# Kernel optimization log

Measured on AMD Instinct MI355X. Metric: run time of the kernel, lower is better.

Reference implementation:

```python
import jax, jax.numpy as jnp
import numpy as np

N, E = 100000, 1600000
IN_C, HID, OUT = 128, 64, 25
EPS = 1e-5


def gcn_conv(x, row, col, W, b):
    # PyG GCNConv: h = x@W; add self-loops; sym-norm D^-1/2 A D^-1/2; + bias
    h = x @ W                                   # [N, F]
    ones = jnp.ones(row.shape[0], h.dtype)
    deg = jax.ops.segment_sum(ones, col, num_segments=N) + 1.0  # +1 self-loop
    dinv = jax.lax.rsqrt(deg)                   # [N]
    norm = dinv[row] * dinv[col]                # [E]
    agg = jax.ops.segment_sum(h[row] * norm[:, None], col, num_segments=N)
    agg = agg + (dinv * dinv)[:, None] * h      # self-loop contribution
    return agg + b


def layer_norm(x, w, b):
    # PyG LayerNorm mode='node': normalize each node over feature dim
    mu = jnp.mean(x, axis=-1, keepdims=True)
    var = jnp.var(x, axis=-1, keepdims=True)
    return (x - mu) * jax.lax.rsqrt(var + EPS) * w + b


def setup_inputs() -> dict:
    key = jax.random.key(0)
    ks = jax.random.split(key, 16)
    x = jax.random.normal(ks[0], (N, IN_C), dtype=jnp.float32)
    edge_index = jax.random.randint(ks[1], (2, E), 0, N, dtype=jnp.int32)

    def glorot(k, shp):
        lim = float(np.sqrt(6.0 / (shp[0] + shp[1])))
        return jax.random.uniform(k, shp, jnp.float32, -lim, lim)

    return {
        "x": x,
        "edge_index": edge_index,
        "W1": glorot(ks[2], (IN_C, HID)), "b1": jnp.zeros((HID,), jnp.float32),
        "W2": glorot(ks[3], (HID, HID)), "b2": jnp.zeros((HID,), jnp.float32),
        "W3": glorot(ks[4], (HID, HID)), "b3": jnp.zeros((HID,), jnp.float32),
        "ln1_w": jnp.ones((HID,), jnp.float32), "ln1_b": jnp.zeros((HID,), jnp.float32),
        "ln2_w": jnp.ones((HID,), jnp.float32), "ln2_b": jnp.zeros((HID,), jnp.float32),
        "ln3_w": jnp.ones((HID,), jnp.float32), "ln3_b": jnp.zeros((HID,), jnp.float32),
        "Wl": glorot(ks[5], (HID, OUT)), "bl": jnp.zeros((OUT,), jnp.float32),
    }


def reference(x, edge_index, W1, b1, W2, b2, W3, b3,
              ln1_w, ln1_b, ln2_w, ln2_b, ln3_w, ln3_b, Wl, bl):
    row, col = edge_index[0], edge_index[1]
    h = jax.nn.relu(layer_norm(gcn_conv(x, row, col, W1, b1), ln1_w, ln1_b))
    h = jax.nn.relu(layer_norm(gcn_conv(h, row, col, W2, b2), ln2_w, ln2_b))
    h = jax.nn.relu(layer_norm(gcn_conv(h, row, col, W3, b3), ln3_w, ln3_b))
    pooled = jnp.mean(h, axis=0)                # [HID]
    return pooled @ Wl + bl                     # [OUT]
```

## Files before the change

kernel.cpp:

```cpp
#include <hip/hip_runtime.h>
#include <hip/hip_bf16.h>

typedef __hip_bfloat16 bf16;
typedef __attribute__((ext_vector_type(8))) short short8;
typedef __attribute__((ext_vector_type(4))) float f32x4;
typedef __attribute__((ext_vector_type(2))) float f32x2;

#define HID 64
#define CAP 4096
#define BSH 7
#define EPB 2048

__device__ __forceinline__ unsigned short f2bfbits(float x){
    union { float f; unsigned u; } c; c.f = x;
    unsigned r = c.u + 0x7fffu + ((c.u >> 16) & 1u);
    return (unsigned short)(r >> 16);
}
__device__ __forceinline__ unsigned char f2fp8(float x){
    unsigned v = __builtin_amdgcn_cvt_pk_fp8_f32(x, x, 0u, false);
    return (unsigned char)(v & 0xffu);
}
template<bool HI>
__device__ __forceinline__ f32x2 cvtpk(unsigned u){
    return __builtin_amdgcn_cvt_pk_f32_fp8(u, HI);
}


__global__ __launch_bounds__(1024) void bin_kernel(const int* __restrict__ row,
                                                   const int* __restrict__ col,
                                                   int E, int NB,
                                                   int* __restrict__ gCur,
                                                   int* __restrict__ binned,
                                                   unsigned char* __restrict__ H8a,
                                                   unsigned char* __restrict__ H8b,
                                                   int N){
    __shared__ int lCnt[1024];
    __shared__ int lOff[1024];
    __shared__ int lGB[1024];
    __shared__ int sPay[EPB];
    __shared__ unsigned short sB[EPB];
    __shared__ int wSum[16];
    int tid = threadIdx.x;
    int lane = tid & 63, wv = tid >> 6;
    if (blockIdx.x == 0 && tid < 32){
        unsigned* za = (unsigned*)(H8a + ((size_t)N << 6));
        unsigned* zb = (unsigned*)(H8b + ((size_t)N << 6));
        if (tid < 16) za[tid] = 0u; else zb[tid - 16] = 0u;
    }
    int e0 = blockIdx.x * EPB;
    int eN = E - e0; if (eN > EPB) eN = EPB;

    lCnt[tid] = 0;
    int cols[2], rows[2];
    #pragma unroll
    for (int k = 0; k < 2; ++k){
        int i = tid + k * 1024;
        bool ok = (i < eN);
        cols[k] = ok ? col[e0 + i] : -1;
        rows[k] = ok ? row[e0 + i] : 0;
    }
    __syncthreads();
    #pragma unroll
    for (int k = 0; k < 2; ++k)
        if (cols[k] >= 0) atomicAdd(&lCnt[cols[k] >> BSH], 1);
    __syncthreads();

    int c = lCnt[tid];
    int inc = c;
    #pragma unroll
    for (int m = 1; m < 64; m <<= 1){
        int t = __shfl_up(inc, m);
        if (lane >= m) inc += t;
    }
    if (lane == 63) wSum[wv] = inc;
    __syncthreads();
    if (wv == 0 && lane < 16){
        int orig = wSum[lane];
        int ws = orig;
        #pragma unroll
        for (int m = 1; m < 16; m <<= 1){
            int t = __shfl_up(ws, m);
            if (lane >= m) ws += t;
        }
        wSum[lane] = ws - orig;
    }
    __syncthreads();
    int excl = inc - c + wSum[wv];
    lOff[tid] = excl;
    if (c){
        int gb = atomicAdd(&gCur[tid], c);
        lGB[tid] = tid * CAP + gb - excl;
    }
    lCnt[tid] = 0;
    __syncthreads();

    #pragma unroll
    for (int k = 0; k < 2; ++k){
        if (cols[k] >= 0){
            int bk = cols[k] >> BSH;
            int rk = atomicAdd(&lCnt[bk], 1);
            int pos = lOff[bk] + rk;
            sPay[pos] = ((cols[k] & 127) << 17) | rows[k];
            sB[pos] = (unsigned short)bk;
        }
    }
    __syncthreads();

    #pragma unroll
    for (int k = 0; k < 2; ++k){
        int i = tid + k * 1024;
        if (i < eN){
            int bk = sB[i];
            int tgt = lGB[bk] + i;
            if (tgt - (bk << 12) < CAP)
                binned[tgt] = sPay[i];
        }
    }
}


__global__ __launch_bounds__(256) void degree_kernel(const int* __restrict__ gCur,
                                                     const int* __restrict__ binned,
                                                     int* __restrict__ col_ptr,
                                                     int* __restrict__ cnt, int N){
    __shared__ int fineCnt[128];
    __shared__ int scW[2];
    int b = blockIdx.x, tid = threadIdx.x;
    int j0 = b * CAP;
    int c = gCur[b];
    if (c > CAP) c = CAP;
    if (tid < 128) fineCnt[tid] = 0;
    __syncthreads();
    for (int i = tid; i < c; i += 256)
        atomicAdd(&fineCnt[binned[j0 + i] >> 17], 1);
    __syncthreads();
    int cf = 0, inc = 0;
    if (tid < 128){
        cf = fineCnt[tid];
        inc = cf;
        #pragma unroll
        for (int m = 1; m < 64; m <<= 1){
            int t = __shfl_up(inc, m);
            if ((tid & 63) >= m) inc += t;
        }
        if ((tid & 63) == 63) scW[tid >> 6] = inc;
    }
    __syncthreads();
    if (tid < 128){
        int off = (tid >= 64) ? scW[0] : 0;
        int node = (b << BSH) + tid;
        if (node < N){
            col_ptr[node] = j0 + off + inc - cf;
            cnt[node] = cf;
        }
    }
}


template<int K, typename T>
__global__ __launch_bounds__(256) void matmul_kernel(const T* __restrict__ act,
                                                     const float* __restrict__ W,
                                                     const int* __restrict__ cnt,
                                                     unsigned char* __restrict__ H8, int N){
    constexpr int KS = K / 32;
    constexpr int RB = 2 * K;
    __shared__ __align__(16) short As[128 * K];
    __shared__ __align__(16) short Wt[64 * K];

    int tid = threadIdx.x;
    int nodeBase = blockIdx.x * 128;

    for (int i = tid; i < K * 64; i += 256){
        int k = i >> 6, c = i & 63;
        unsigned short b = f2bfbits(W[i]);
        int byte = c * RB + ((2 * k) ^ ((c & 7) << 4));
        *(short*)((char*)Wt + byte) = (short)b;
    }
    constexpr int OPR = K / 8;
    for (int i = tid; i < 128 * OPR; i += 256){
        int node = i / OPR, oct = i % OPR;
        int n = nodeBase + node;
        short8 v = (short8)0;
        if (n < N){
            if constexpr (sizeof(T) == 4){
                const float4* xp = (const float4*)&act[(size_t)n * K + oct * 8];
                float4 a = xp[0], b = xp[1];
                v[0] = (short)f2bfbits(a.x); v[1] = (short)f2bfbits(a.y);
                v[2] = (short)f2bfbits(a.z); v[3] = (short)f2bfbits(a.w);
                v[4] = (short)f2bfbits(b.x); v[5] = (short)f2bfbits(b.y);
                v[6] = (short)f2bfbits(b.z); v[7] = (short)f2bfbits(b.w);
            } else {
                v = *(const short8*)&act[(size_t)n * K + oct * 8];
            }
        }
        int byte = node * RB + ((oct * 16) ^ ((node & 7) << 4));
        *(short8*)((char*)As + byte) = v;
    }
    __syncthreads();

    int wv = tid >> 6, l = tid & 63;
    int lr = l & 15, lg = l >> 4;

    short8 bfr[KS][4];
    #pragma unroll
    for (int ks = 0; ks < KS; ++ks)
        #pragma unroll
        for (int t = 0; t < 4; ++t){
            int c = t * 16 + lr;
            int byte = c * RB + ((ks * 64 + lg * 16) ^ ((c & 7) << 4));
            bfr[ks][t] = *(const short8*)((const char*)Wt + byte);
        }

    #pragma unroll
    for (int nt = 0; nt < 2; ++nt){
        int nb = wv * 32 + nt * 16;
        int node = nb + lr;
        short8 af[KS];
        #pragma unroll
        for (int ks = 0; ks < KS; ++ks){
            int byte = node * RB + ((ks * 64 + lg * 16) ^ ((node & 7) << 4));
            af[ks] = *(const short8*)((const char*)As + byte);
        }
        f32x4 acc[4] = {(f32x4)0.f, (f32x4)0.f, (f32x4)0.f, (f32x4)0.f};
        #pragma unroll
        for (int ks = 0; ks < KS; ++ks)
            #pragma unroll
            for (int t = 0; t < 4; ++t)
                acc[t] = __builtin_amdgcn_mfma_f32_16x16x32_bf16(af[ks], bfr[ks][t], acc[t], 0, 0, 0);
        #pragma unroll
        for (int r = 0; r < 4; ++r){
            int n = nodeBase + nb + lg * 4 + r;
            if (n < N){
                float dv = rsqrtf((float)cnt[n] + 1.0f);
                #pragma unroll
                for (int t = 0; t < 4; ++t)
                    H8[((size_t)(unsigned)n << 6) + t * 16 + lr] = f2fp8(acc[t][r] * dv);
            }
        }
    }
}


__global__ __launch_bounds__(512) void agg_sort_kernel(const unsigned char* __restrict__ H8in,
                                                       const int* __restrict__ cnt,
                                                       const int* __restrict__ gCur,
                                                       const int* __restrict__ binned,
                                                       const int* __restrict__ col_ptr,
                                                       int* __restrict__ csr_row,
                                                       const float* __restrict__ bias,
                                                       const float* __restrict__ lnw,
                                                       const float* __restrict__ lnb,
                                                       const float* __restrict__ Wn,
                                                       unsigned char* __restrict__ H8out,
                                                       int N){
    __shared__ int sCsr[CAP];
    __shared__ __align__(16) short ybuf[8192];
    __shared__ __align__(16) short Wt[4096];
    __shared__ int fineCur[128];
    __shared__ float sdv[128];
    int b = blockIdx.x, tid = threadIdx.x;
    int wid = tid >> 6, l = tid & 63;
    int g = l >> 2, s = l & 3;
    int nodeBase = b << BSH;
    int n = nodeBase + wid * 16 + g;
    bool valid = (n < N);
    int nc = valid ? n : nodeBase;

    int j0g = b * CAP;
    int cntB = gCur[b];
    if (cntB > CAP) cntB = CAP;

    for (int i = tid; i < 4096; i += 512){
        int k = i >> 6, c = i & 63;
        unsigned short bb = f2bfbits(Wn[i]);
        int byte = c * 128 + ((2 * k) ^ ((c & 7) << 4));
        *(short*)((char*)Wt + byte) = (short)bb;
    }
    if (tid < 128){
        int node = nodeBase + tid;
        fineCur[tid] = (node < N) ? (col_ptr[node] - j0g) : 0;
    }
    __syncthreads();

    for (int i = tid; i < cntB; i += 512){
        int w = binned[j0g + i];
        int pos = atomicAdd(&fineCur[w >> 17], 1);
        sCsr[pos] = w & 0x1FFFF;
    }
    __syncthreads();
    for (int i = tid; i < cntB; i += 512) csr_row[j0g + i] = sCsr[i];

    int deg = valid ? cnt[nc] : 0;
    int p = valid ? (col_ptr[nc] - j0g) : 0;
    unsigned soff = (unsigned)(s << 4);
    const char* Hb = (const char*)H8in;
    uint4 us = *(const uint4*)(Hb + ((((unsigned)nc) << 6) | soff));

    int mdeg = deg;
    mdeg = max(mdeg, __shfl_xor(mdeg, 4));
    mdeg = max(mdeg, __shfl_xor(mdeg, 8));
    mdeg = max(mdeg, __shfl_xor(mdeg, 16));
    mdeg = max(mdeg, __shfl_xor(mdeg, 32));

    f32x2 a0 = {0.f,0.f}, a1 = {0.f,0.f}, a2 = {0.f,0.f}, a3 = {0.f,0.f};
    f32x2 a4 = {0.f,0.f}, a5 = {0.f,0.f}, a6 = {0.f,0.f}, a7 = {0.f,0.f};
#define ACC4(u) { a0 += cvtpk<false>((u).x); a1 += cvtpk<true>((u).x); \
                  a2 += cvtpk<false>((u).y); a3 += cvtpk<true>((u).y); \
                  a4 += cvtpk<false>((u).z); a5 += cvtpk<true>((u).z); \
                  a6 += cvtpk<false>((u).w); a7 += cvtpk<true>((u).w); }
    for (int i = 0; i < mdeg; i += 4){
        int r0 = (i     < deg) ? sCsr[p + i    ] : N;
        int r1 = (i + 1 < deg) ? sCsr[p + i + 1] : N;
        int r2 = (i + 2 < deg) ? sCsr[p + i + 2] : N;
        int r3 = (i + 3 < deg) ? sCsr[p + i + 3] : N;
        uint4 u0 = *(const uint4*)(Hb + ((((unsigned)r0) << 6) | soff));
        uint4 u1 = *(const uint4*)(Hb + ((((unsigned)r1) << 6) | soff));
        uint4 u2 = *(const uint4*)(Hb + ((((unsigned)r2) << 6) | soff));
        uint4 u3 = *(const uint4*)(Hb + ((((unsigned)r3) << 6) | soff));
        ACC4(u0) ACC4(u1) ACC4(u2) ACC4(u3)
    }
#undef ACC4
    a0 += cvtpk<false>(us.x); a1 += cvtpk<true>(us.x);
    a2 += cvtpk<false>(us.y); a3 += cvtpk<true>(us.y);
    a4 += cvtpk<false>(us.z); a5 += cvtpk<true>(us.z);
    a6 += cvtpk<false>(us.w); a7 += cvtpk<true>(us.w);

    float dv = rsqrtf((float)deg + 1.0f);
    float acc16[16] = { a0.x, a0.y, a1.x, a1.y, a2.x, a2.y, a3.x, a3.y,
                        a4.x, a4.y, a5.x, a5.y, a6.x, a6.y, a7.x, a7.y };
    float v[16], y[16];
    float4 bq[4], wq[4], cq[4];
    #pragma unroll
    for (int q = 0; q < 4; ++q){
        bq[q] = ((const float4*)bias)[(s << 2) + q];
        wq[q] = ((const float4*)lnw)[(s << 2) + q];
        cq[q] = ((const float4*)lnb)[(s << 2) + q];
    }
    #pragma unroll
    for (int j = 0; j < 16; ++j)
        v[j] = fmaf(dv, acc16[j], ((const float*)&bq[j >> 2])[j & 3]);
    float sum = 0.f;
    #pragma unroll
    for (int j = 0; j < 16; ++j) sum += v[j];
    sum += __shfl_xor(sum, 1); sum += __shfl_xor(sum, 2);
    float mu = sum * (1.0f / 64.0f);
    float var = 0.f;
    #pragma unroll
    for (int j = 0; j < 16; ++j){ float d = v[j] - mu; var = fmaf(d, d, var); }
    var += __shfl_xor(var, 1); var += __shfl_xor(var, 2);
    float rstd = rsqrtf(var * (1.0f / 64.0f) + 1e-5f);
    #pragma unroll
    for (int j = 0; j < 16; ++j){
        float d = (v[j] - mu) * rstd;
        y[j] = fmaxf(fmaf(d, ((const float*)&wq[j >> 2])[j & 3],
                             ((const float*)&cq[j >> 2])[j & 3]), 0.0f);
    }

    if (s == 0) sdv[(wid << 4) + g] = dv;
    char* yb = (char*)ybuf;
    int base = (wid << 11) + (g << 7);
    int sw = (g & 7) << 4;
    short8 ya, yz;
    #pragma unroll
    for (int j = 0; j < 8; ++j){ ya[j] = (short)f2bfbits(y[j]); yz[j] = (short)f2bfbits(y[8 + j]); }
    *(short8*)(yb + base + (((s << 5)     ) ^ sw)) = ya;
    *(short8*)(yb + base + (((s << 5) + 16) ^ sw)) = yz;

    int lr = l & 15, lg = l >> 4;
    short8 bfr[2][4];
    #pragma unroll
    for (int ks = 0; ks < 2; ++ks)
        #pragma unroll
        for (int t = 0; t < 4; ++t){
            int c = t * 16 + lr;
            int byte = c * 128 + ((((ks << 2) + lg) << 4) ^ ((c & 7) << 4));
            bfr[ks][t] = *(const short8*)((const char*)Wt + byte);
        }
    short8 af[2];
    #pragma unroll
    for (int ks = 0; ks < 2; ++ks){
        int byte = (wid << 11) + lr * 128 + ((((ks << 2) + lg) << 4) ^ ((lr & 7) << 4));
        af[ks] = *(const short8*)(yb + byte);
    }
    f32x4 acc[4] = {(f32x4)0.f, (f32x4)0.f, (f32x4)0.f, (f32x4)0.f};
    #pragma unroll
    for (int ks = 0; ks < 2; ++ks)
        #pragma unroll
        for (int t = 0; t < 4; ++t)
            acc[t] = __builtin_amdgcn_mfma_f32_16x16x32_bf16(af[ks], bfr[ks][t], acc[t], 0, 0, 0);
    #pragma unroll
    for (int r = 0; r < 4; ++r){
        int nn = nodeBase + (wid << 4) + (lg << 2) + r;
        if (nn < N){
            float dv2 = sdv[(wid << 4) + (lg << 2) + r];
            #pragma unroll
            for (int t = 0; t < 4; ++t)
                H8out[((size_t)(unsigned)nn << 6) + t * 16 + lr] = f2fp8(acc[t][r] * dv2);
        }
    }
}


template<bool POOL>
__global__ __launch_bounds__(256) void agg_kernel(const unsigned char* __restrict__ H8in,
                                                  const int* __restrict__ cnt,
                                                  const int* __restrict__ col_ptr,
                                                  const int* __restrict__ csr_row,
                                                  const float* __restrict__ bias,
                                                  const float* __restrict__ lnw,
                                                  const float* __restrict__ lnb,
                                                  const float* __restrict__ Wn,
                                                  unsigned char* __restrict__ H8out,
                                                  float* __restrict__ pooledRep, int N){
    __shared__ int sIdx[CAP];
    __shared__ __align__(16) short ybuf[POOL ? 8 : 4096];
    __shared__ __align__(16) short Wt[POOL ? 8 : 4096];
    __shared__ float sp[POOL ? 256 : 4];
    __shared__ float sdv[64];
    int tid = threadIdx.x;
    int wid = tid >> 6, l = tid & 63;
    int g = l >> 2, s = l & 3;
    int nodeBase = blockIdx.x * 64;
    int n = nodeBase + wid * 16 + g;
    bool valid = (n < N);
    int nc = valid ? n : nodeBase;

    int lastN = nodeBase + 63; if (lastN > N - 1) lastN = N - 1;
    int jlo = col_ptr[nodeBase];
    int jhi = col_ptr[lastN] + cnt[lastN];
    int cntR = jhi - jlo;

    int deg = valid ? cnt[nc] : 0;
    int p = (valid ? col_ptr[nc] : jlo) - jlo;

    for (int i = tid; i < cntR; i += 256) sIdx[i] = csr_row[jlo + i];
    if (!POOL){
        for (int i = tid; i < 4096; i += 256){
            int k = i >> 6, c = i & 63;
            unsigned short bb = f2bfbits(Wn[i]);
            int byte = c * 128 + ((2 * k) ^ ((c & 7) << 4));
            *(short*)((char*)Wt + byte) = (short)bb;
        }
    }
    __syncthreads();

    unsigned soff = (unsigned)(s << 4);
    const char* Hb = (const char*)H8in;
    uint4 us = *(const uint4*)(Hb + ((((unsigned)nc) << 6) | soff));

    int mdeg = deg;
    mdeg = max(mdeg, __shfl_xor(mdeg, 4));
    mdeg = max(mdeg, __shfl_xor(mdeg, 8));
    mdeg = max(mdeg, __shfl_xor(mdeg, 16));
    mdeg = max(mdeg, __shfl_xor(mdeg, 32));

    f32x2 a0 = {0.f,0.f}, a1 = {0.f,0.f}, a2 = {0.f,0.f}, a3 = {0.f,0.f};
    f32x2 a4 = {0.f,0.f}, a5 = {0.f,0.f}, a6 = {0.f,0.f}, a7 = {0.f,0.f};
#define ACC4(u) { a0 += cvtpk<false>((u).x); a1 += cvtpk<true>((u).x); \
                  a2 += cvtpk<false>((u).y); a3 += cvtpk<true>((u).y); \
                  a4 += cvtpk<false>((u).z); a5 += cvtpk<true>((u).z); \
                  a6 += cvtpk<false>((u).w); a7 += cvtpk<true>((u).w); }
    for (int i = 0; i < mdeg; i += 4){
        int r0 = (i     < deg) ? sIdx[p + i    ] : N;
        int r1 = (i + 1 < deg) ? sIdx[p + i + 1] : N;
        int r2 = (i + 2 < deg) ? sIdx[p + i + 2] : N;
        int r3 = (i + 3 < deg) ? sIdx[p + i + 3] : N;
        uint4 u0 = *(const uint4*)(Hb + ((((unsigned)r0) << 6) | soff));
        uint4 u1 = *(const uint4*)(Hb + ((((unsigned)r1) << 6) | soff));
        uint4 u2 = *(const uint4*)(Hb + ((((unsigned)r2) << 6) | soff));
        uint4 u3 = *(const uint4*)(Hb + ((((unsigned)r3) << 6) | soff));
        ACC4(u0) ACC4(u1) ACC4(u2) ACC4(u3)
    }
#undef ACC4
    a0 += cvtpk<false>(us.x); a1 += cvtpk<true>(us.x);
    a2 += cvtpk<false>(us.y); a3 += cvtpk<true>(us.y);
    a4 += cvtpk<false>(us.z); a5 += cvtpk<true>(us.z);
    a6 += cvtpk<false>(us.w); a7 += cvtpk<true>(us.w);

    float dv = rsqrtf((float)deg + 1.0f);
    float acc16[16] = { a0.x, a0.y, a1.x, a1.y, a2.x, a2.y, a3.x, a3.y,
                        a4.x, a4.y, a5.x, a5.y, a6.x, a6.y, a7.x, a7.y };
    float v[16], y[16];
    float4 bq[4], wq[4], cq[4];
    #pragma unroll
    for (int q = 0; q < 4; ++q){
        bq[q] = ((const float4*)bias)[(s << 2) + q];
        wq[q] = ((const float4*)lnw)[(s << 2) + q];
        cq[q] = ((const float4*)lnb)[(s << 2) + q];
    }
    #pragma unroll
    for (int j = 0; j < 16; ++j)
        v[j] = fmaf(dv, acc16[j], ((const float*)&bq[j >> 2])[j & 3]);
    float sum = 0.f;
    #pragma unroll
    for (int j = 0; j < 16; ++j) sum += v[j];
    sum += __shfl_xor(sum, 1); sum += __shfl_xor(sum, 2);
    float mu = sum * (1.0f / 64.0f);
    float var = 0.f;
    #pragma unroll
    for (int j = 0; j < 16; ++j){ float d = v[j] - mu; var = fmaf(d, d, var); }
    var += __shfl_xor(var, 1); var += __shfl_xor(var, 2);
    float rstd = rsqrtf(var * (1.0f / 64.0f) + 1e-5f);
    #pragma unroll
    for (int j = 0; j < 16; ++j){
        float d = (v[j] - mu) * rstd;
        y[j] = fmaxf(fmaf(d, ((const float*)&wq[j >> 2])[j & 3],
                             ((const float*)&cq[j >> 2])[j & 3]), 0.0f);
    }

    if (POOL){
        #pragma unroll
        for (int j = 0; j < 16; ++j){
            float z = valid ? y[j] : 0.f;
            z += __shfl_xor(z, 4); z += __shfl_xor(z, 8);
            z += __shfl_xor(z, 16); z += __shfl_xor(z, 32);
            y[j] = z;
        }
        if (l < 4){
            #pragma unroll
            for (int q = 0; q < 4; ++q)
                ((float4*)sp)[wid * 16 + (s << 2) + q] =
                    make_float4(y[4*q], y[4*q+1], y[4*q+2], y[4*q+3]);
        }
        __syncthreads();
        if (tid < 64){
            float t = sp[tid] + sp[64 + tid] + sp[128 + tid] + sp[192 + tid];
            atomicAdd(&pooledRep[(blockIdx.x & 63) * 64 + tid], t);
        }
    } else {
        if (s == 0) sdv[(wid << 4) + g] = dv;
        char* yb = (char*)ybuf;
        int base = (wid << 11) + (g << 7);
        int sw = (g & 7) << 4;
        short8 ya, yz;
        #pragma unroll
        for (int j = 0; j < 8; ++j){ ya[j] = (short)f2bfbits(y[j]); yz[j] = (short)f2bfbits(y[8 + j]); }
        *(short8*)(yb + base + (((s << 5)     ) ^ sw)) = ya;
        *(short8*)(yb + base + (((s << 5) + 16) ^ sw)) = yz;

        int lr = l & 15, lg = l >> 4;
        short8 bfr[2][4];
        #pragma unroll
        for (int ks = 0; ks < 2; ++ks)
            #pragma unroll
            for (int t = 0; t < 4; ++t){
                int c = t * 16 + lr;
                int byte = c * 128 + ((((ks << 2) + lg) << 4) ^ ((c & 7) << 4));
                bfr[ks][t] = *(const short8*)((const char*)Wt + byte);
            }
        short8 af[2];
        #pragma unroll
        for (int ks = 0; ks < 2; ++ks){
            int byte = (wid << 11) + lr * 128 + ((((ks << 2) + lg) << 4) ^ ((lr & 7) << 4));
            af[ks] = *(const short8*)(yb + byte);
        }
        f32x4 acc[4] = {(f32x4)0.f, (f32x4)0.f, (f32x4)0.f, (f32x4)0.f};
        #pragma unroll
        for (int ks = 0; ks < 2; ++ks)
            #pragma unroll
            for (int t = 0; t < 4; ++t)
                acc[t] = __builtin_amdgcn_mfma_f32_16x16x32_bf16(af[ks], bfr[ks][t], acc[t], 0, 0, 0);
        #pragma unroll
        for (int r = 0; r < 4; ++r){
            int nn = nodeBase + (wid << 4) + (lg << 2) + r;
            if (nn < N){
                float dv2 = sdv[(wid << 4) + (lg << 2) + r];
                #pragma unroll
                for (int t = 0; t < 4; ++t)
                    H8out[((size_t)(unsigned)nn << 6) + t * 16 + lr] = f2fp8(acc[t][r] * dv2);
            }
        }
    }
}


__global__ __launch_bounds__(64) void final_kernel(const float* __restrict__ pooledRep,
                                                   const float* __restrict__ Wl,
                                                   const float* __restrict__ bl,
                                                   float* __restrict__ outp, float invN){
    __shared__ float pooled[64];
    int t = threadIdx.x;
    float s = 0.f;
    #pragma unroll 8
    for (int r = 0; r < 64; ++r) s += pooledRep[r * 64 + t];
    pooled[t] = s;
    __syncthreads();
    if (t < 25){
        float acc = bl[t];
        #pragma unroll 8
        for (int f = 0; f < HID; ++f)
            acc = fmaf(pooled[f] * invN, Wl[f * 25 + t], acc);
        outp[t] = acc;
    }
}


static inline size_t alignup(size_t x){ return (x + 255) & ~(size_t)255; }

extern "C" void kernel_launch(void* const* d_in, const int* in_sizes, int n_in,
                              void* d_out, int out_size, void* d_ws, size_t ws_size,
                              hipStream_t stream) {
    const float* x   = (const float*)d_in[0];
    const int*   ei  = (const int*)d_in[1];
    const float* W1  = (const float*)d_in[2];
    const float* b1  = (const float*)d_in[3];
    const float* W2  = (const float*)d_in[4];
    const float* b2  = (const float*)d_in[5];
    const float* W3  = (const float*)d_in[6];
    const float* b3  = (const float*)d_in[7];
    const float* ln1w = (const float*)d_in[8];
    const float* ln1b = (const float*)d_in[9];
    const float* ln2w = (const float*)d_in[10];
    const float* ln2b = (const float*)d_in[11];
    const float* ln3w = (const float*)d_in[12];
    const float* ln3b = (const float*)d_in[13];
    const float* Wl  = (const float*)d_in[14];
    const float* bl  = (const float*)d_in[15];

    const int N = in_sizes[0] / 128;
    const int E = in_sizes[1] / 2;
    const int NB = (N + 127) >> BSH;
    const int* row = ei;
    const int* col = ei + E;

    char* p = (char*)d_ws;
    int*   gCur      = (int*)p;   p += alignup((size_t)NB * 4);
    float* pooledRep = (float*)p; p += alignup(64 * 64 * 4);
    size_t zeroBytes = (size_t)((char*)p - (char*)gCur);
    int*   binned    = (int*)p;   p += alignup((size_t)NB * CAP * 4);
    int*   csr_row   = (int*)p;   p += alignup((size_t)NB * CAP * 4);
    int*   col_ptr   = (int*)p;   p += alignup((size_t)N * 4);
    int*   cnt       = (int*)p;   p += alignup((size_t)N * 4);
    unsigned char* H8a = (unsigned char*)p; p += alignup(((size_t)N + 1) * HID);
    unsigned char* H8b = (unsigned char*)p; p += alignup(((size_t)N + 1) * HID);

    hipMemsetAsync(gCur, 0, zeroBytes, stream);

    int gB = (E + EPB - 1) / EPB;
    int gM = (N + 127) / 128;
    int gA = (N + 63) / 64;

    bin_kernel<<<gB, 1024, 0, stream>>>(row, col, E, NB, gCur, binned, H8a, H8b, N);
    degree_kernel<<<NB, 256, 0, stream>>>(gCur, binned, col_ptr, cnt, N);

    matmul_kernel<128, float><<<gM, 256, 0, stream>>>(x, W1, cnt, H8a, N);
    agg_sort_kernel<<<NB, 512, 0, stream>>>(H8a, cnt, gCur, binned, col_ptr, csr_row,
                                            b1, ln1w, ln1b, W2, H8b, N);
    agg_kernel<false><<<gA, 256, 0, stream>>>(H8b, cnt, col_ptr, csr_row,
                                              b2, ln2w, ln2b, W3, H8a, pooledRep, N);
    agg_kernel<true><<<gA, 256, 0, stream>>>(H8a, cnt, col_ptr, csr_row,
                                             b3, ln3w, ln3b, nullptr, nullptr, pooledRep, N);

    final_kernel<<<1, 64, 0, stream>>>(pooledRep, Wl, bl, (float*)d_out, 1.0f / (float)N);
}
```

Before: 239.4 us.

## Sort nodes by degree within each 64-node group to balance wavefront work

The degree kernel now ranks each 64-node group by in-degree and writes a permutation. The aggregation kernels assign nodes to lanes through this permutation, so the 16 nodes handled by one wavefront have similar degrees and the loop bound (max degree in the wave) wastes fewer iterations. Output rows are scattered back through a shared-memory copy of the permutation. This adds a 64-step shuffle ranking and an extra indirection, and makes H8 reads and writes less contiguous.

Result: slower. 248.1 us (+3.6%).

```diff
diff --git a/kernel.cpp b/kernel.cpp
--- a/kernel.cpp
+++ b/kernel.cpp
@@ -122,7 +122,8 @@
 __global__ __launch_bounds__(256) void degree_kernel(const int* __restrict__ gCur,
                                                      const int* __restrict__ binned,
                                                      int* __restrict__ col_ptr,
-                                                     int* __restrict__ cnt, int N){
+                                                     int* __restrict__ cnt,
+                                                     int* __restrict__ perm, int N){
     __shared__ int fineCnt[128];
     __shared__ int scW[2];
     int b = blockIdx.x, tid = threadIdx.x;
@@ -147,12 +148,21 @@
     }
     __syncthreads();
     if (tid < 128){
+        int lane = tid & 63, w = tid >> 6;
         int off = (tid >= 64) ? scW[0] : 0;
         int node = (b << BSH) + tid;
-        if (node < N){
+        bool v = (node < N);
+        if (v){
             col_ptr[node] = j0 + off + inc - cf;
             cnt[node] = cf;
         }
+        int key = v ? cf : 0x7fffffff;
+        int rank = 0;
+        for (int j = 0; j < 64; ++j){
+            int kj = __shfl(key, j);
+            rank += (kj < key) || (kj == key && j < lane);
+        }
+        perm[(b << BSH) + (w << 6) + rank] = v ? node : N;
     }
 }
 
@@ -246,6 +256,7 @@
                                                        const int* __restrict__ gCur,
                                                        const int* __restrict__ binned,
                                                        const int* __restrict__ col_ptr,
+                                                       const int* __restrict__ perm,
                                                        int* __restrict__ csr_row,
                                                        const float* __restrict__ bias,
                                                        const float* __restrict__ lnw,
@@ -258,13 +269,11 @@
     __shared__ __align__(16) short Wt[4096];
     __shared__ int fineCur[128];
     __shared__ float sdv[128];
+    __shared__ int sperm[128];
     int b = blockIdx.x, tid = threadIdx.x;
     int wid = tid >> 6, l = tid & 63;
     int g = l >> 2, s = l & 3;
     int nodeBase = b << BSH;
-    int n = nodeBase + wid * 16 + g;
-    bool valid = (n < N);
-    int nc = valid ? n : nodeBase;
 
     int j0g = b * CAP;
     int cntB = gCur[b];
@@ -290,8 +299,12 @@
     __syncthreads();
     for (int i = tid; i < cntB; i += 512) csr_row[j0g + i] = sCsr[i];
 
-    int deg = valid ? cnt[nc] : 0;
-    int p = valid ? (col_ptr[nc] - j0g) : 0;
+    int node = perm[nodeBase + (wid << 4) + g];
+    bool valid = (node < N);
+    int nc = valid ? node : N;
+    int deg = valid ? cnt[node] : 0;
+    int p = valid ? (col_ptr[node] - j0g) : 0;
+
     unsigned soff = (unsigned)(s << 4);
     const char* Hb = (const char*)H8in;
     uint4 us = *(const uint4*)(Hb + ((((unsigned)nc) << 6) | soff));
@@ -356,7 +369,7 @@
                              ((const float*)&cq[j >> 2])[j & 3]), 0.0f);
     }
 
-    if (s == 0) sdv[(wid << 4) + g] = dv;
+    if (s == 0){ sdv[(wid << 4) + g] = dv; sperm[(wid << 4) + g] = nc; }
     char* yb = (char*)ybuf;
     int base = (wid << 11) + (g << 7);
     int sw = (g & 7) << 4;
@@ -390,9 +403,10 @@
             acc[t] = __builtin_amdgcn_mfma_f32_16x16x32_bf16(af[ks], bfr[ks][t], acc[t], 0, 0, 0);
     #pragma unroll
     for (int r = 0; r < 4; ++r){
-        int nn = nodeBase + (wid << 4) + (lg << 2) + r;
+        int idx = (wid << 4) + (lg << 2) + r;
+        int nn = sperm[idx];
         if (nn < N){
-            float dv2 = sdv[(wid << 4) + (lg << 2) + r];
+            float dv2 = sdv[idx];
             #pragma unroll
             for (int t = 0; t < 4; ++t)
                 H8out[((size_t)(unsigned)nn << 6) + t * 16 + lr] = f2fp8(acc[t][r] * dv2);
@@ -406,6 +420,7 @@
                                                   const int* __restrict__ cnt,
                                                   const int* __restrict__ col_ptr,
                                                   const int* __restrict__ csr_row,
+                                                  const int* __restrict__ perm,
                                                   const float* __restrict__ bias,
                                                   const float* __restrict__ lnw,
                                                   const float* __restrict__ lnb,
@@ -417,21 +432,22 @@
     __shared__ __align__(16) short Wt[POOL ? 8 : 4096];
     __shared__ float sp[POOL ? 256 : 4];
     __shared__ float sdv[64];
+    __shared__ int sperm[64];
     int tid = threadIdx.x;
     int wid = tid >> 6, l = tid & 63;
     int g = l >> 2, s = l & 3;
     int nodeBase = blockIdx.x * 64;
-    int n = nodeBase + wid * 16 + g;
-    bool valid = (n < N);
-    int nc = valid ? n : nodeBase;
 
     int lastN = nodeBase + 63; if (lastN > N - 1) lastN = N - 1;
     int jlo = col_ptr[nodeBase];
     int jhi = col_ptr[lastN] + cnt[lastN];
     int cntR = jhi - jlo;
 
-    int deg = valid ? cnt[nc] : 0;
-    int p = (valid ? col_ptr[nc] : jlo) - jlo;
+    int node = perm[nodeBase + (wid << 4) + g];
+    bool valid = (node < N);
+    int nc = valid ? node : N;
+    int deg = valid ? cnt[node] : 0;
+    int p = valid ? (col_ptr[node] - jlo) : 0;
 
     for (int i = tid; i < cntR; i += 256) sIdx[i] = csr_row[jlo + i];
     if (!POOL){
@@ -528,7 +544,7 @@
             atomicAdd(&pooledRep[(blockIdx.x & 63) * 64 + tid], t);
         }
     } else {
-        if (s == 0) sdv[(wid << 4) + g] = dv;
+        if (s == 0){ sdv[(wid << 4) + g] = dv; sperm[(wid << 4) + g] = nc; }
         char* yb = (char*)ybuf;
         int base = (wid << 11) + (g << 7);
         int sw = (g & 7) << 4;
@@ -562,9 +578,10 @@
                 acc[t] = __builtin_amdgcn_mfma_f32_16x16x32_bf16(af[ks], bfr[ks][t], acc[t], 0, 0, 0);
         #pragma unroll
         for (int r = 0; r < 4; ++r){
-            int nn = nodeBase + (wid << 4) + (lg << 2) + r;
+            int idx = (wid << 4) + (lg << 2) + r;
+            int nn = sperm[idx];
             if (nn < N){
-                float dv2 = sdv[(wid << 4) + (lg << 2) + r];
+                float dv2 = sdv[idx];
                 #pragma unroll
                 for (int t = 0; t < 4; ++t)
                     H8out[((size_t)(unsigned)nn << 6) + t * 16 + lr] = f2fp8(acc[t][r] * dv2);
@@ -631,6 +648,7 @@
     int*   csr_row   = (int*)p;   p += alignup((size_t)NB * CAP * 4);
     int*   col_ptr   = (int*)p;   p += alignup((size_t)N * 4);
     int*   cnt       = (int*)p;   p += alignup((size_t)N * 4);
+    int*   perm      = (int*)p;   p += alignup((size_t)NB * 128 * 4);
     unsigned char* H8a = (unsigned char*)p; p += alignup(((size_t)N + 1) * HID);
     unsigned char* H8b = (unsigned char*)p; p += alignup(((size_t)N + 1) * HID);
 
@@ -641,14 +659,14 @@
     int gA = (N + 63) / 64;
 
     bin_kernel<<<gB, 1024, 0, stream>>>(row, col, E, NB, gCur, binned, H8a, H8b, N);
-    degree_kernel<<<NB, 256, 0, stream>>>(gCur, binned, col_ptr, cnt, N);
+    degree_kernel<<<NB, 256, 0, stream>>>(gCur, binned, col_ptr, cnt, perm, N);
 
     matmul_kernel<128, float><<<gM, 256, 0, stream>>>(x, W1, cnt, H8a, N);
-    agg_sort_kernel<<<NB, 512, 0, stream>>>(H8a, cnt, gCur, binned, col_ptr, csr_row,
+    agg_sort_kernel<<<NB, 512, 0, stream>>>(H8a, cnt, gCur, binned, col_ptr, perm, csr_row,
                                             b1, ln1w, ln1b, W2, H8b, N);
-    agg_kernel<false><<<gA, 256, 0, stream>>>(H8b, cnt, col_ptr, csr_row,
+    agg_kernel<false><<<gA, 256, 0, stream>>>(H8b, cnt, col_ptr, csr_row, perm,
                                               b2, ln2w, ln2b, W3, H8a, pooledRep, N);
-    agg_kernel<true><<<gA, 256, 0, stream>>>(H8a, cnt, col_ptr, csr_row,
+    agg_kernel<true><<<gA, 256, 0, stream>>>(H8a, cnt, col_ptr, csr_row, perm,
                                              b3, ln3w, ln3b, nullptr, nullptr, pooledRep, N);
 
     final_kernel<<<1, 64, 0, stream>>>(pooledRep, Wl, bl, (float*)d_out, 1.0f / (float)N);
```
